# Performance work log

Measured on AMD Instinct MI355X. Metric: run time of the kernel, lower is better.

Reference implementation:

```python
import jax, jax.numpy as jnp
import numpy as np

D = 256   # hidden_dim
N = 1024  # total nodes
NP = 384  # paratope nodes
NE = 384  # epitope nodes
NC = 14   # atom channels


def setup_inputs() -> dict:
    key = jax.random.key(0)
    ks = jax.random.split(key, 24)
    s = 1.0 / np.sqrt(D)
    s3 = 1.0 / np.sqrt(3 * D)
    w = lambda k, shape, sc: (jax.random.normal(k, shape, jnp.float32) * sc)
    z = lambda: jnp.zeros((D,), jnp.float32)
    return {
        "H": w(ks[0], (N, D), 1.0),
        "X": w(ks[1], (N, NC, 3), 1.0),
        "paratope_mask": jnp.zeros((N,), bool).at[:NP].set(True),
        "epitope_mask": jnp.zeros((N,), bool).at[NP:NP + NE].set(True),
        "res_w1": w(ks[2], (1, D), 1.0), "res_b1": z(),
        "res_w2": w(ks[3], (D, D), s), "res_b2": z(),
        "atom_w1": w(ks[4], (1, D), 1.0), "atom_b1": z(),
        "atom_w2": w(ks[5], (D, D), s), "atom_b2": z(),
        "sim_weight": jnp.float32(0.5),
        "int_w1": w(ks[6], (3 * D, D), s3), "int_b1": z(),
        "int_w2": w(ks[7], (D, D), s), "int_b2": z(),
        "wl": w(ks[8], (D, D), s),
        "wr": w(ks[9], (D, D), s),
        "wg_w": w(ks[10], (D, D), s), "wg_b": z(),
        "wq_w": w(ks[11], (D, D), s), "wq_b": z(),
        "wk_w": w(ks[12], (D, D), s), "wk_b": z(),
        "wv_w": w(ks[13], (D, D), s), "wv_b": z(),
    }


def _mlp2(x, w1, b1, w2, b2):
    return jax.nn.silu(x @ w1 + b1) @ w2 + b2


def reference(H, X, paratope_mask, epitope_mask,
              res_w1, res_b1, res_w2, res_b2,
              atom_w1, atom_b1, atom_w2, atom_b2,
              sim_weight,
              int_w1, int_b1, int_w2, int_b2,
              wl, wr, wg_w, wg_b, wq_w, wq_b, wk_w, wk_b, wv_w, wv_b):
    p_idx = jnp.nonzero(paratope_mask, size=NP)[0]
    e_idx = jnp.nonzero(epitope_mask, size=NE)[0]
    Hp = H[p_idx]                      # [NP, D]
    He = H[e_idx]                      # [NE, D]
    Xp_ca = X[p_idx, 1]                # [NP, 3] (CA atom)
    Xe_ca = X[e_idx, 1]                # [NE, 3]

    dX = Xp_ca[:, None, :] - Xe_ca[None, :, :]         # [NP, NE, 3]
    S = jnp.sum(dX * dX, axis=-1, keepdims=True)       # [NP, NE, 1]
    # original computes S_residue and S_atom with identical formula
    S_res = _mlp2(S, res_w1, res_b1, res_w2, res_b2)
    S_atom = _mlp2(S, atom_w1, atom_b1, atom_w2, atom_b2)
    wmix = jax.nn.sigmoid(sim_weight)
    S_comb = wmix * S_res + (1.0 - wmix) * S_atom      # [NP, NE, D]

    Hp_e = jnp.broadcast_to(Hp[:, None, :], (NP, NE, D))
    He_e = jnp.broadcast_to(He[None, :, :], (NP, NE, D))
    Z_in = jnp.concatenate([Hp_e, He_e, S_comb], axis=-1)  # [NP, NE, 3D]
    Z = _mlp2(Z_in, int_w1, int_b1, int_w2, int_b2)        # [NP, NE, D]

    I = (Hp @ wl)[:, None, :] * (He @ wr)[None, :, :]      # outer-product interaction
    gate = jax.nn.sigmoid(Z @ wg_w + wg_b)
    f_tri = gate * I

    Q = Z @ wq_w + wq_b
    K = Z @ wk_w + wk_b
    V = Z @ wv_w + wv_b
    scores = jnp.einsum('ped,pfd->pef', Q, K) / (D ** 0.5)  # [NP, NE, NE]
    A = jax.nn.softmax(scores, axis=-1)
    f_att = jnp.einsum('pef,pfd->ped', A, V)

    H_tri = f_tri + f_att                                   # [NP, NE, D]
    return H.at[p_idx].set(H_tri.mean(axis=1))
```

## Files before the change

### kernel.cpp

```cpp
#include <hip/hip_runtime.h>

#define NPAR 384
#define NEPI 384
#define DD   256
#define NTAB 4096
#define SMAX 96.0f
#define SDELTA (SMAX / NTAB)
#define SINVD (NTAB / SMAX)

using bf16x8 = __bf16 __attribute__((ext_vector_type(8)));
using bf16x2 = __bf16 __attribute__((ext_vector_type(2)));
using f32x4  = float __attribute__((ext_vector_type(4)));

#if defined(__has_builtin)
#if __has_builtin(__builtin_amdgcn_cvt_pk_bf16_f32)
#define HAVE_PK_BF16 1
#endif
#if __has_builtin(__builtin_amdgcn_rcpf)
#define HAVE_RCPF 1
#endif
#endif

__device__ __forceinline__ float fastrcp(float x) {
#ifdef HAVE_RCPF
  return __builtin_amdgcn_rcpf(x);
#else
  return 1.0f / x;
#endif
}
__device__ __forceinline__ float sigm(float x) { return fastrcp(1.0f + __expf(-x)); }
__device__ __forceinline__ float silu(float x) { return x * fastrcp(1.0f + __expf(-x)); }
__device__ __forceinline__ unsigned short f2bf(float f) {
  unsigned u = __float_as_uint(f);
  u += 0x7fffu + ((u >> 16) & 1u);
  return (unsigned short)(u >> 16);
}
__device__ __forceinline__ float bf2f(unsigned u16) {
  return __uint_as_float(u16 << 16);
}
__device__ __forceinline__ uint2 pack4(float a, float b, float c, float d) {
  uint2 r;
#ifdef HAVE_PK_BF16
  bf16x2 lo = __builtin_amdgcn_cvt_pk_bf16_f32(a, b);
  bf16x2 hi = __builtin_amdgcn_cvt_pk_bf16_f32(c, d);
  r.x = __builtin_bit_cast(unsigned, lo);
  r.y = __builtin_bit_cast(unsigned, hi);
#else
  r.x = (unsigned)f2bf(a) | ((unsigned)f2bf(b) << 16);
  r.y = (unsigned)f2bf(c) | ((unsigned)f2bf(d) << 16);
#endif
  return r;
}

__device__ __forceinline__ void store_packed(unsigned short* __restrict__ wp,
                                             int slot, int k, int n, float v) {
  const int ks = k >> 5, lhi = (k >> 3) & 3, j = k & 7;
  const int tile = n >> 4, llo = n & 15;
  const int lane = lhi * 16 + llo;
  wp[slot * 65536 + (((ks * 16 + tile) * 64 + lane) << 3) + j] = f2bf(v);
}


__global__ void prep_kernel(
    const float* __restrict__ H, const float* __restrict__ wl,
    const float* __restrict__ wr, const float* __restrict__ int_w1,
    const float* __restrict__ res_w2, const float* __restrict__ atom_w2,
    const float* __restrict__ res_b2, const float* __restrict__ atom_b2,
    const float* __restrict__ int_b1, const float* __restrict__ simw,
    const float* __restrict__ wq_b, const float* __restrict__ wk_w,
    const float* __restrict__ wq_w, const float* __restrict__ int_w2,
    const float* __restrict__ wg_w,
    float* __restrict__ Hpl, float* __restrict__ Her,
    float* __restrict__ P1, float* __restrict__ P2,
    float* __restrict__ cvec, float* __restrict__ gv,
    unsigned short* __restrict__ wpack) {
  __shared__ float sbuf[1024];
  const int b = blockIdx.x, t = threadIdx.x;
  if (b < 256) {
    const bool isMa = b >= 128;
    const int i0 = (b & 127) * 2;
    const float wmix = 1.0f / (1.0f + __expf(-simw[0]));
    const float sc = isMa ? (1.0f - wmix) : wmix;
    const float* W2 = isMa ? atom_w2 : res_w2;
    sbuf[t] = W2[i0 * 256 + t];
    sbuf[256 + t] = W2[(i0 + 1) * 256 + t];
    __syncthreads();
    float a0 = 0.f, a1 = 0.f;
#pragma unroll 8
    for (int k = 0; k < 256; ++k) {
      const float w = int_w1[(512 + k) * 256 + t];
      a0 = fmaf(sbuf[k], w, a0);
      a1 = fmaf(sbuf[256 + k], w, a1);
    }
    const int slot = isMa ? 1 : 0;
    store_packed(wpack, slot, i0, t, a0 * sc);
    store_packed(wpack, slot, i0 + 1, t, a1 * sc);
  } else if (b == 256) {
    const float wmix = 1.0f / (1.0f + __expf(-simw[0]));
    float acc = int_b1[t];
#pragma unroll 8
    for (int k = 0; k < 256; ++k) {
      float bm = wmix * res_b2[k] + (1.0f - wmix) * atom_b2[k];
      acc += bm * int_w1[(512 + k) * 256 + t];
    }
    cvec[t] = acc;
  } else if (b < 321) {
    const int lane = t & 63, w = t >> 6;
    const int d = (b - 257) * 4 + w;
    float acc = 0.f;
#pragma unroll
    for (int i = 0; i < 4; ++i) {
      const int c = i * 64 + lane;
      acc += wk_w[d * 256 + c] * wq_b[c];
    }
    acc += __shfl_xor(acc, 1);
    acc += __shfl_xor(acc, 2);
    acc += __shfl_xor(acc, 4);
    acc += __shfl_xor(acc, 8);
    acc += __shfl_xor(acc, 16);
    acc += __shfl_xor(acc, 32);
    if (lane == 0) gv[d] = acc;
  } else if (b < 577) {
    const int r = b - 321;
    sbuf[t] = wq_w[r * 256 + t];
    __syncthreads();
    const float* wkrow = wk_w + t * 256;
    float a0 = 0.f, a1 = 0.f, a2 = 0.f, a3 = 0.f;
#pragma unroll 4
    for (int k = 0; k < 256; k += 4) {
      const f32x4 wv4 = *reinterpret_cast<const f32x4*>(&wkrow[k]);
      a0 = fmaf(sbuf[k + 0], wv4[0], a0);
      a1 = fmaf(sbuf[k + 1], wv4[1], a1);
      a2 = fmaf(sbuf[k + 2], wv4[2], a2);
      a3 = fmaf(sbuf[k + 3], wv4[3], a3);
    }
    store_packed(wpack, 4, r, t, (a0 + a1) + (a2 + a3));
  } else if (b < 961) {
    const int idx = b - 577;
    const int seg = idx / 96, r0 = (idx % 96) * 4;
    const float* A;
    const float* B;
    float* C;
    switch (seg) {
      case 0:  A = H + r0 * 256;            B = wl;              C = Hpl + r0 * 256; break;
      case 1:  A = H + (NPAR + r0) * 256;   B = wr;              C = Her + r0 * 256; break;
      case 2:  A = H + r0 * 256;            B = int_w1;          C = P1 + r0 * 256;  break;
      default: A = H + (NPAR + r0) * 256;   B = int_w1 + 65536;  C = P2 + r0 * 256;  break;
    }
#pragma unroll
    for (int j = 0; j < 4; ++j) sbuf[j * 256 + t] = A[j * 256 + t];
    __syncthreads();
    float a0 = 0.f, a1 = 0.f, a2 = 0.f, a3 = 0.f;
#pragma unroll 8
    for (int k = 0; k < 256; ++k) {
      const float bv = B[k * 256 + t];
      a0 = fmaf(sbuf[k], bv, a0);
      a1 = fmaf(sbuf[256 + k], bv, a1);
      a2 = fmaf(sbuf[512 + k], bv, a2);
      a3 = fmaf(sbuf[768 + k], bv, a3);
    }
    C[t] = a0;
    C[256 + t] = a1;
    C[512 + t] = a2;
    C[768 + t] = a3;
  } else {
    const int idx = (b - 961) * 256 + t;
    const int m = idx >> 16;
    const int r = idx & 65535;
    const int chunk = r >> 9;
    const int lane = (r >> 3) & 63;
    const int j = r & 7;
    const int k = (chunk >> 4) * 32 + (lane >> 4) * 8 + j;
    const int n = (chunk & 15) * 16 + (lane & 15);
    const float* src = (m == 0) ? int_w2 : wg_w;
    wpack[(2 + m) * 65536 + r] = f2bf(src[k * 256 + n]);
  }
}


__device__ __forceinline__ void zero_acc4(f32x4 (&acc)[4][4]) {
#pragma unroll
  for (int mt = 0; mt < 4; ++mt)
#pragma unroll
    for (int nt = 0; nt < 4; ++nt)
      acc[mt][nt] = (f32x4){0.f, 0.f, 0.f, 0.f};
}

__device__ __forceinline__ void gemm4(f32x4 (&acc)[4][4],
                                      const unsigned short* __restrict__ wp,
                                      const unsigned short* ub, int lane, int wv) {
  const int l15 = lane & 15, l4 = lane >> 4;
#pragma unroll
  for (int ks = 0; ks < 8; ++ks) {
    bf16x8 a[4];
#pragma unroll
    for (int mt = 0; mt < 4; ++mt)
      a[mt] = *reinterpret_cast<const bf16x8*>(wp + ((ks * 16 + wv * 4 + mt) * 64 + lane) * 8);
    __builtin_amdgcn_s_setprio(1);
#pragma unroll
    for (int nt = 0; nt < 4; ++nt) {
      bf16x8 b = *reinterpret_cast<const bf16x8*>(ub + (nt * 16 + l15) * 264 + ks * 32 + l4 * 8);
#pragma unroll
      for (int mt = 0; mt < 4; ++mt)
        acc[mt][nt] = __builtin_amdgcn_mfma_f32_16x16x32_bf16(a[mt], b, acc[mt][nt], 0, 0, 0);
    }
    __builtin_amdgcn_s_setprio(0);
  }
}

__device__ __forceinline__ void fill_u(unsigned short* ub, const float* Sv,
                                       const float* __restrict__ w1,
                                       const float* __restrict__ b1, int t) {
  const int dg = t & 31, rb = t >> 5;
  const f32x4 w1a = *reinterpret_cast<const f32x4*>(&w1[dg * 8]);
  const f32x4 w1b = *reinterpret_cast<const f32x4*>(&w1[dg * 8 + 4]);
  const f32x4 b1a = *reinterpret_cast<const f32x4*>(&b1[dg * 8]);
  const f32x4 b1b = *reinterpret_cast<const f32x4*>(&b1[dg * 8 + 4]);
#pragma unroll
  for (int i = 0; i < 8; ++i) {
    const int e = rb + i * 8;
    const float s = Sv[e];
    uint2 lo = pack4(silu(fmaf(s, w1a[0], b1a[0])), silu(fmaf(s, w1a[1], b1a[1])),
                     silu(fmaf(s, w1a[2], b1a[2])), silu(fmaf(s, w1a[3], b1a[3])));
    uint2 hi = pack4(silu(fmaf(s, w1b[0], b1b[0])), silu(fmaf(s, w1b[1], b1b[1])),
                     silu(fmaf(s, w1b[2], b1b[2])), silu(fmaf(s, w1b[3], b1b[3])));
    uint4 pk = {lo.x, lo.y, hi.x, hi.y};
    *reinterpret_cast<uint4*>(&ub[e * 264 + dg * 8]) = pk;
  }
}


__global__ __launch_bounds__(256, 3) void tab_kernel(
    const float* __restrict__ res_w1, const float* __restrict__ res_b1,
    const float* __restrict__ atom_w1, const float* __restrict__ atom_b1,
    const unsigned short* __restrict__ wpack, float* __restrict__ tabF) {
  __shared__ __align__(16) unsigned short ubuf[64 * 264];
  __shared__ float Sv[64];
  const int t = threadIdx.x, lane = t & 63, wv = t >> 6;
  const int l15 = lane & 15, l4 = lane >> 4;
  const int n0 = blockIdx.x * 64;
  if (t < 64) Sv[t] = (n0 + t) * SDELTA;
  __syncthreads();
  f32x4 acc[4][4];
  zero_acc4(acc);
  fill_u(ubuf, Sv, res_w1, res_b1, t);
  __syncthreads();
  gemm4(acc, wpack + 0 * 65536, ubuf, lane, wv);
  __syncthreads();
  fill_u(ubuf, Sv, atom_w1, atom_b1, t);
  __syncthreads();
  gemm4(acc, wpack + 1 * 65536, ubuf, lane, wv);
#pragma unroll
  for (int mt = 0; mt < 4; ++mt) {
    const int d = wv * 64 + mt * 16 + l4 * 4;
#pragma unroll
    for (int nt = 0; nt < 4; ++nt) {
      const int n = n0 + nt * 16 + l15;
      *reinterpret_cast<f32x4*>(&tabF[n * 256 + d]) = acc[mt][nt];
    }
  }
}


__global__ __launch_bounds__(256, 4) void pair_kernel(
    const float* __restrict__ Xg, const float* __restrict__ tabF,
    const float* __restrict__ int_b2, const float* __restrict__ wg_b,
    const unsigned short* __restrict__ wpack, const float* __restrict__ cvec,
    const float* __restrict__ P1, const float* __restrict__ P2,
    const float* __restrict__ Hpl, const float* __restrict__ Her,
    float* __restrict__ ftri, unsigned short* __restrict__ Zsw) {
  __shared__ __align__(16) unsigned short ubuf[64 * 264];
  __shared__ float Sv[64];
  __shared__ float pc[DD];
  const int t = threadIdx.x, lane = t & 63, wv = t >> 6;
  const int l15 = lane & 15, l4 = lane >> 4;
  const int wg = (blockIdx.x & 7) * 288 + (blockIdx.x >> 3);
  const int p = wg / 6, cc = wg % 6, e0 = cc * 64;
  const int d0 = wv * 64;

  if (t < 64) {
    const int e = e0 + t;
    float dx = Xg[p * 42 + 3] - Xg[(NPAR + e) * 42 + 3];
    float dy = Xg[p * 42 + 4] - Xg[(NPAR + e) * 42 + 4];
    float dz = Xg[p * 42 + 5] - Xg[(NPAR + e) * 42 + 5];
    Sv[t] = dx * dx + dy * dy + dz * dz;
  }
  pc[t] = P1[p * DD + t] + cvec[t];
  __syncthreads();

  {
    const int dg = t & 31, rb = t >> 5;
    const f32x4 pca = *reinterpret_cast<const f32x4*>(&pc[dg * 8]);
    const f32x4 pcb = *reinterpret_cast<const f32x4*>(&pc[dg * 8 + 4]);
#pragma unroll
    for (int i = 0; i < 8; ++i) {
      const int e = rb + i * 8;
      float sv = Sv[e] * SINVD;
      int idx = (int)sv;
      idx = idx > (NTAB - 2) ? (NTAB - 2) : idx;
      const float fr = sv - (float)idx;
      const f32x4 t0a = *reinterpret_cast<const f32x4*>(&tabF[idx * 256 + dg * 8]);
      const f32x4 t0b = *reinterpret_cast<const f32x4*>(&tabF[idx * 256 + dg * 8 + 4]);
      const f32x4 t1a = *reinterpret_cast<const f32x4*>(&tabF[(idx + 1) * 256 + dg * 8]);
      const f32x4 t1b = *reinterpret_cast<const f32x4*>(&tabF[(idx + 1) * 256 + dg * 8 + 4]);
      const f32x4 p2a = *reinterpret_cast<const f32x4*>(&P2[(e0 + e) * DD + dg * 8]);
      const f32x4 p2b = *reinterpret_cast<const f32x4*>(&P2[(e0 + e) * DD + dg * 8 + 4]);
      float z0 = fmaf(fr, t1a[0] - t0a[0], t0a[0]) + pca[0] + p2a[0];
      float z1 = fmaf(fr, t1a[1] - t0a[1], t0a[1]) + pca[1] + p2a[1];
      float z2 = fmaf(fr, t1a[2] - t0a[2], t0a[2]) + pca[2] + p2a[2];
      float z3 = fmaf(fr, t1a[3] - t0a[3], t0a[3]) + pca[3] + p2a[3];
      float z4 = fmaf(fr, t1b[0] - t0b[0], t0b[0]) + pcb[0] + p2b[0];
      float z5 = fmaf(fr, t1b[1] - t0b[1], t0b[1]) + pcb[1] + p2b[1];
      float z6 = fmaf(fr, t1b[2] - t0b[2], t0b[2]) + pcb[2] + p2b[2];
      float z7 = fmaf(fr, t1b[3] - t0b[3], t0b[3]) + pcb[3] + p2b[3];
      uint2 lo = pack4(silu(z0), silu(z1), silu(z2), silu(z3));
      uint2 hi = pack4(silu(z4), silu(z5), silu(z6), silu(z7));
      uint4 pk = {lo.x, lo.y, hi.x, hi.y};
      *reinterpret_cast<uint4*>(&ubuf[e * 264 + dg * 8]) = pk;
    }
  }
  __syncthreads();

  f32x4 acc[4][4];
  zero_acc4(acc);
  gemm4(acc, wpack + 2 * 65536, ubuf, lane, wv);
  __syncthreads();
#pragma unroll
  for (int mt = 0; mt < 4; ++mt) {
    const int d = d0 + mt * 16 + l4 * 4;
    const f32x4 bb = *reinterpret_cast<const f32x4*>(&int_b2[d]);
#pragma unroll
    for (int nt = 0; nt < 4; ++nt) {
      const int e = nt * 16 + l15;
      *reinterpret_cast<uint2*>(&ubuf[e * 264 + d]) =
          pack4(acc[mt][nt][0] + bb[0], acc[mt][nt][1] + bb[1],
                acc[mt][nt][2] + bb[2], acc[mt][nt][3] + bb[3]);
    }
  }
  __syncthreads();

  {
    unsigned short* Zd = Zsw + (size_t)p * 98304 + (size_t)(cc * 4 + wv) * 4096 + lane * 8;
#pragma unroll
    for (int ks = 0; ks < 8; ++ks) {
      *reinterpret_cast<uint4*>(Zd + ks * 512) =
          *reinterpret_cast<const uint4*>(&ubuf[(wv * 16 + l15) * 264 + ks * 32 + l4 * 8]);
    }
  }

  zero_acc4(acc);
  gemm4(acc, wpack + 3 * 65536, ubuf, lane, wv);
#pragma unroll
  for (int mt = 0; mt < 4; ++mt) {
    const int d = d0 + mt * 16 + l4 * 4;
    const f32x4 bb = *reinterpret_cast<const f32x4*>(&wg_b[d]);
    const f32x4 hl = *reinterpret_cast<const f32x4*>(&Hpl[p * DD + d]);
    f32x4 fs = (f32x4){0.f, 0.f, 0.f, 0.f};
#pragma unroll
    for (int nt = 0; nt < 4; ++nt) {
      const int e = e0 + nt * 16 + l15;
      const f32x4 hr = *reinterpret_cast<const f32x4*>(&Her[e * DD + d]);
#pragma unroll
      for (int r = 0; r < 4; ++r)
        fs[r] += sigm(acc[mt][nt][r] + bb[r]) * hr[r];
    }
#pragma unroll
    for (int r = 0; r < 4; ++r) {
      float v = fs[r] * hl[r];
      v += __shfl_xor(v, 1);
      v += __shfl_xor(v, 2);
      v += __shfl_xor(v, 4);
      v += __shfl_xor(v, 8);
      if (l15 == 0) atomicAdd(&ftri[p * DD + d + r], v);
    }
  }
}


__global__ __launch_bounds__(256, 4) void attn_kernel(
    const unsigned short* __restrict__ Zsw, const float* __restrict__ gv,
    const unsigned short* __restrict__ wpack, float* __restrict__ cbufg) {
  __shared__ __align__(16) unsigned short Tc[32 * 264];
  __shared__ float red[128];
  __shared__ float red2[128];
  const int t = threadIdx.x, lane = t & 63, wv = t >> 6;
  const int l15 = lane & 15, l4 = lane >> 4;
  const int xcd = blockIdx.x & 7, inner = blockIdx.x >> 3;
  const int p = (inner / 12) * 8 + xcd, c = inner % 12;
  const unsigned short* Zsp = Zsw + (size_t)p * 98304;
  const unsigned short* wqk = wpack + 4 * 65536;

  {
    f32x4 ta[4][2];
#pragma unroll
    for (int mt = 0; mt < 4; ++mt)
#pragma unroll
      for (int nt = 0; nt < 2; ++nt) ta[mt][nt] = (f32x4){0.f, 0.f, 0.f, 0.f};
    const unsigned short* Tb = Zsp + (size_t)(c * 2) * 4096 + lane * 8;
    bf16x8 bcur[2], bnxt[2];
#pragma unroll
    for (int nt = 0; nt < 2; ++nt)
      bcur[nt] = *reinterpret_cast<const bf16x8*>(Tb + nt * 4096);
#pragma unroll
    for (int ks = 0; ks < 8; ++ks) {
      if (ks < 7) {
#pragma unroll
        for (int nt = 0; nt < 2; ++nt)
          bnxt[nt] = *reinterpret_cast<const bf16x8*>(Tb + nt * 4096 + (ks + 1) * 512);
      }
      bf16x8 a[4];
#pragma unroll
      for (int mt = 0; mt < 4; ++mt)
        a[mt] = *reinterpret_cast<const bf16x8*>(wqk + ((ks * 16 + wv * 4 + mt) * 64 + lane) * 8);
      __builtin_amdgcn_s_setprio(1);
#pragma unroll
      for (int nt = 0; nt < 2; ++nt)
#pragma unroll
        for (int mt = 0; mt < 4; ++mt)
          ta[mt][nt] = __builtin_amdgcn_mfma_f32_16x16x32_bf16(a[mt], bcur[nt], ta[mt][nt], 0, 0, 0);
      __builtin_amdgcn_s_setprio(0);
      if (ks < 7) {
#pragma unroll
        for (int nt = 0; nt < 2; ++nt) bcur[nt] = bnxt[nt];
      }
    }
#pragma unroll
    for (int mt = 0; mt < 4; ++mt) {
      const int d = wv * 64 + mt * 16 + l4 * 4;
      const f32x4 gq = *reinterpret_cast<const f32x4*>(&gv[d]);
#pragma unroll
      for (int nt = 0; nt < 2; ++nt) {
        const int e = nt * 16 + l15;
        *reinterpret_cast<uint2*>(&Tc[e * 264 + d]) =
            pack4((ta[mt][nt][0] + gq[0]) * 0.0625f, (ta[mt][nt][1] + gq[1]) * 0.0625f,
                  (ta[mt][nt][2] + gq[2]) * 0.0625f, (ta[mt][nt][3] + gq[3]) * 0.0625f);
      }
    }
  }
  __syncthreads();

  f32x4 sc[2][6];
#pragma unroll
  for (int mt = 0; mt < 2; ++mt)
#pragma unroll
    for (int s = 0; s < 6; ++s) sc[mt][s] = (f32x4){0.f, 0.f, 0.f, 0.f};

  {
    const unsigned short* Sb = Zsp + (size_t)wv * 4096 + lane * 8;
    bf16x8 b0[3], b1[3];
#pragma unroll
    for (int j = 0; j < 3; ++j)
      b0[j] = *reinterpret_cast<const bf16x8*>(Sb + j * 16384);
#pragma unroll
    for (int ks = 0; ks < 8; ++ks) {
#pragma unroll
      for (int j = 0; j < 3; ++j)
        b1[j] = *reinterpret_cast<const bf16x8*>(Sb + (3 + j) * 16384 + ks * 512);
      bf16x8 a[2];
#pragma unroll
      for (int mt = 0; mt < 2; ++mt)
        a[mt] = *reinterpret_cast<const bf16x8*>(&Tc[(mt * 16 + l15) * 264 + ks * 32 + l4 * 8]);
      __builtin_amdgcn_s_setprio(1);
#pragma unroll
      for (int j = 0; j < 3; ++j)
#pragma unroll
        for (int mt = 0; mt < 2; ++mt)
          sc[mt][j] = __builtin_amdgcn_mfma_f32_16x16x32_bf16(a[mt], b0[j], sc[mt][j], 0, 0, 0);
      __builtin_amdgcn_s_setprio(0);
      if (ks < 7) {
#pragma unroll
        for (int j = 0; j < 3; ++j)
          b0[j] = *reinterpret_cast<const bf16x8*>(Sb + j * 16384 + (ks + 1) * 512);
      }
      __builtin_amdgcn_s_setprio(1);
#pragma unroll
      for (int j = 0; j < 3; ++j)
#pragma unroll
        for (int mt = 0; mt < 2; ++mt)
          sc[mt][3 + j] = __builtin_amdgcn_mfma_f32_16x16x32_bf16(a[mt], b1[j], sc[mt][3 + j], 0, 0, 0);
      __builtin_amdgcn_s_setprio(0);
    }
  }

  float rmax[2][4];
#pragma unroll
  for (int mt = 0; mt < 2; ++mt) {
#pragma unroll
    for (int r = 0; r < 4; ++r) {
      float m = -1e30f;
#pragma unroll
      for (int s = 0; s < 6; ++s) m = fmaxf(m, sc[mt][s][r]);
      m = fmaxf(m, __shfl_xor(m, 1));
      m = fmaxf(m, __shfl_xor(m, 2));
      m = fmaxf(m, __shfl_xor(m, 4));
      m = fmaxf(m, __shfl_xor(m, 8));
      rmax[mt][r] = m;
    }
  }
  if (l15 == 0) {
#pragma unroll
    for (int mt = 0; mt < 2; ++mt)
#pragma unroll
      for (int r = 0; r < 4; ++r)
        red[wv * 32 + mt * 16 + l4 * 4 + r] = rmax[mt][r];
  }
  __syncthreads();
#pragma unroll
  for (int mt = 0; mt < 2; ++mt) {
#pragma unroll
    for (int r = 0; r < 4; ++r) {
      const int row = mt * 16 + l4 * 4 + r;
      rmax[mt][r] = fmaxf(fmaxf(red[row], red[32 + row]), fmaxf(red[64 + row], red[96 + row]));
    }
  }

  float rsum[2][4];
#pragma unroll
  for (int mt = 0; mt < 2; ++mt) {
#pragma unroll
    for (int r = 0; r < 4; ++r) {
      float sSum = 0.f;
#pragma unroll
      for (int s = 0; s < 6; ++s) {
        float e = __expf(sc[mt][s][r] - rmax[mt][r]);
        sc[mt][s][r] = e;
        sSum += e;
      }
      sSum += __shfl_xor(sSum, 1);
      sSum += __shfl_xor(sSum, 2);
      sSum += __shfl_xor(sSum, 4);
      sSum += __shfl_xor(sSum, 8);
      rsum[mt][r] = sSum;
    }
  }
  if (l15 == 0) {
#pragma unroll
    for (int mt = 0; mt < 2; ++mt)
#pragma unroll
      for (int r = 0; r < 4; ++r)
        red2[wv * 32 + mt * 16 + l4 * 4 + r] = rsum[mt][r];
  }
  __syncthreads();
  float rinv[2][4];
#pragma unroll
  for (int mt = 0; mt < 2; ++mt) {
#pragma unroll
    for (int r = 0; r < 4; ++r) {
      const int row = mt * 16 + l4 * 4 + r;
      rinv[mt][r] = fastrcp(red2[row] + red2[32 + row] + red2[64 + row] + red2[96 + row]);
    }
  }

#pragma unroll
  for (int s = 0; s < 6; ++s) {
    float v = 0.f;
#pragma unroll
    for (int mt = 0; mt < 2; ++mt)
#pragma unroll
      for (int r = 0; r < 4; ++r)
        v += sc[mt][s][r] * rinv[mt][r];
    v += __shfl_xor(v, 16);
    v += __shfl_xor(v, 32);
    if (lane < 16)
      atomicAdd(&cbufg[p * NEPI + (s * 4 + wv) * 16 + lane], v);
  }
}


__global__ __launch_bounds__(256) void outa_kernel(
    const unsigned short* __restrict__ Zsw, const float* __restrict__ cbufg,
    float* __restrict__ ubufg) {
  __shared__ float cb[128];
  __shared__ float part[16][257];
  const int p = blockIdx.x / 3, th = blockIdx.x % 3, g0 = th * 8;
  const int t = threadIdx.x;
  const int lane = t & 63, wv = t >> 6;
  const int l15 = lane & 15, l4 = lane >> 4;
  if (t < 128) cb[t] = cbufg[p * NEPI + g0 * 16 + t];
  __syncthreads();
  const unsigned short* Zsp = Zsw + (size_t)p * 98304;
  float a16[16];
#pragma unroll
  for (int j = 0; j < 16; ++j) a16[j] = 0.f;
#pragma unroll
  for (int gr = 0; gr < 8; ++gr) {
    const int grp = g0 + gr;
    const float w = cb[gr * 16 + l15];
    const uint4 z0 = *reinterpret_cast<const uint4*>(Zsp + grp * 4096 + wv * 512 + lane * 8);
    const uint4 z1 = *reinterpret_cast<const uint4*>(Zsp + grp * 4096 + (wv + 4) * 512 + lane * 8);
    a16[0] = fmaf(w, bf2f(z0.x & 0xffffu), a16[0]);
    a16[1] = fmaf(w, bf2f(z0.x >> 16), a16[1]);
    a16[2] = fmaf(w, bf2f(z0.y & 0xffffu), a16[2]);
    a16[3] = fmaf(w, bf2f(z0.y >> 16), a16[3]);
    a16[4] = fmaf(w, bf2f(z0.z & 0xffffu), a16[4]);
    a16[5] = fmaf(w, bf2f(z0.z >> 16), a16[5]);
    a16[6] = fmaf(w, bf2f(z0.w & 0xffffu), a16[6]);
    a16[7] = fmaf(w, bf2f(z0.w >> 16), a16[7]);
    a16[8]  = fmaf(w, bf2f(z1.x & 0xffffu), a16[8]);
    a16[9]  = fmaf(w, bf2f(z1.x >> 16), a16[9]);
    a16[10] = fmaf(w, bf2f(z1.y & 0xffffu), a16[10]);
    a16[11] = fmaf(w, bf2f(z1.y >> 16), a16[11]);
    a16[12] = fmaf(w, bf2f(z1.z & 0xffffu), a16[12]);
    a16[13] = fmaf(w, bf2f(z1.z >> 16), a16[13]);
    a16[14] = fmaf(w, bf2f(z1.w & 0xffffu), a16[14]);
    a16[15] = fmaf(w, bf2f(z1.w >> 16), a16[15]);
  }
#pragma unroll
  for (int j = 0; j < 8; ++j) part[l15][wv * 32 + l4 * 8 + j] = a16[j];
#pragma unroll
  for (int j = 0; j < 8; ++j) part[l15][128 + wv * 32 + l4 * 8 + j] = a16[8 + j];
  __syncthreads();
  float uu = 0.f;
#pragma unroll
  for (int g = 0; g < 16; ++g) uu += part[g][t];
  atomicAdd(&ubufg[p * DD + t], uu);
}


__global__ __launch_bounds__(256) void out2_kernel(
    const float* __restrict__ ubufg, const float* __restrict__ ftri,
    const float* __restrict__ wvw, const float* __restrict__ wvb,
    float* __restrict__ out) {
  __shared__ float u[DD];
  const int p = blockIdx.x, t = threadIdx.x;
  u[t] = ubufg[p * DD + t];
  __syncthreads();
  float acc = ftri[p * DD + t] + 384.0f * wvb[t];
#pragma unroll 8
  for (int d = 0; d < DD; ++d)
    acc = fmaf(u[d], wvw[d * DD + t], acc);
  out[p * DD + t] = acc * (1.0f / 384.0f);
}


extern "C" void kernel_launch(void* const* d_in, const int* in_sizes, int n_in,
                              void* d_out, int out_size, void* d_ws, size_t ws_size,
                              hipStream_t stream) {
  (void)in_sizes; (void)n_in; (void)out_size; (void)ws_size;
  const float* H = (const float*)d_in[0];
  const float* X = (const float*)d_in[1];
  const float* res_w1 = (const float*)d_in[4];
  const float* res_b1 = (const float*)d_in[5];
  const float* res_w2 = (const float*)d_in[6];
  const float* res_b2 = (const float*)d_in[7];
  const float* atom_w1 = (const float*)d_in[8];
  const float* atom_b1 = (const float*)d_in[9];
  const float* atom_w2 = (const float*)d_in[10];
  const float* atom_b2 = (const float*)d_in[11];
  const float* simw = (const float*)d_in[12];
  const float* int_w1 = (const float*)d_in[13];
  const float* int_b1 = (const float*)d_in[14];
  const float* int_w2 = (const float*)d_in[15];
  const float* int_b2 = (const float*)d_in[16];
  const float* wl = (const float*)d_in[17];
  const float* wr = (const float*)d_in[18];
  const float* wg_w = (const float*)d_in[19];
  const float* wg_b = (const float*)d_in[20];
  const float* wq_w = (const float*)d_in[21];
  const float* wq_b = (const float*)d_in[22];
  const float* wk_w = (const float*)d_in[23];
  const float* wv_w = (const float*)d_in[25];
  const float* wv_b = (const float*)d_in[26];

  char* ws = (char*)d_ws;
  unsigned short* wpack = (unsigned short*)(ws + 0);
  float* cvec  = (float*)(ws + 655360);
  float* gv    = (float*)(ws + 656384);
  float* P1    = (float*)(ws + 657408);
  float* P2    = (float*)(ws + 1050624);
  float* Hpl   = (float*)(ws + 1443840);
  float* Her   = (float*)(ws + 1837056);
  float* ftri  = (float*)(ws + 2230272);
  float* cbufg = (float*)(ws + 2623488);
  float* ubufg = (float*)(ws + 3213312);
  unsigned short* Zsw = (unsigned short*)(ws + 3606528);
  float* tabF  = (float*)(ws + 79104000);

  hipMemsetAsync(ftri, 0, 393216 + 589824 + 393216, stream);
  prep_kernel<<<1473, 256, 0, stream>>>(H, wl, wr, int_w1, res_w2, atom_w2,
                                        res_b2, atom_b2, int_b1, simw, wq_b, wk_w,
                                        wq_w, int_w2, wg_w,
                                        Hpl, Her, P1, P2, cvec, gv, wpack);
  tab_kernel<<<NTAB / 64, 256, 0, stream>>>(res_w1, res_b1, atom_w1, atom_b1, wpack, tabF);
  pair_kernel<<<2304, 256, 0, stream>>>(X, tabF, int_b2, wg_b, wpack, cvec,
                                        P1, P2, Hpl, Her, ftri, Zsw);
  attn_kernel<<<4608, 256, 0, stream>>>(Zsw, gv, wpack, cbufg);
  outa_kernel<<<1152, 256, 0, stream>>>(Zsw, cbufg, ubufg);
  out2_kernel<<<384, 256, 0, stream>>>(ubufg, ftri, wv_w, wv_b, (float*)d_out);
  hipMemcpyAsync((float*)d_out + NPAR * DD, H + NPAR * DD,
                 (1024 - NPAR) * DD * sizeof(float), hipMemcpyDeviceToDevice, stream);
}
```

Measured before the change: 312.0 us.

## Prefetch full next k-slice in attention, drop pc smem staging, move memcpy first

The attention score loop now prefetches all six B fragments for the next k-step into a second register set and issues all twelve MFMAs per step together, replacing the split half-prefetch scheme. In pair_kernel, the per-row P1+cvec vector is read straight from global memory into registers instead of being staged through shared memory. The tail device-to-device copy of untouched H rows is moved to the start of the stream. Together these aim to hide load latency and trim shared memory use, at the cost of more VGPRs, which may reduce occupancy.

```diff
diff --git a/kernel.cpp b/kernel.cpp
--- a/kernel.cpp
+++ b/kernel.cpp
@@ -271,7 +271,6 @@
     float* __restrict__ ftri, unsigned short* __restrict__ Zsw) {
   __shared__ __align__(16) unsigned short ubuf[64 * 264];
   __shared__ float Sv[64];
-  __shared__ float pc[DD];
   const int t = threadIdx.x, lane = t & 63, wv = t >> 6;
   const int l15 = lane & 15, l4 = lane >> 4;
   const int wg = (blockIdx.x & 7) * 288 + (blockIdx.x >> 3);
@@ -285,13 +284,16 @@
     float dz = Xg[p * 42 + 5] - Xg[(NPAR + e) * 42 + 5];
     Sv[t] = dx * dx + dy * dy + dz * dz;
   }
-  pc[t] = P1[p * DD + t] + cvec[t];
   __syncthreads();
 
   {
     const int dg = t & 31, rb = t >> 5;
-    const f32x4 pca = *reinterpret_cast<const f32x4*>(&pc[dg * 8]);
-    const f32x4 pcb = *reinterpret_cast<const f32x4*>(&pc[dg * 8 + 4]);
+    const f32x4 p1a = *reinterpret_cast<const f32x4*>(&P1[p * DD + dg * 8]);
+    const f32x4 p1b = *reinterpret_cast<const f32x4*>(&P1[p * DD + dg * 8 + 4]);
+    const f32x4 cva = *reinterpret_cast<const f32x4*>(&cvec[dg * 8]);
+    const f32x4 cvb = *reinterpret_cast<const f32x4*>(&cvec[dg * 8 + 4]);
+    const f32x4 pca = p1a + cva;
+    const f32x4 pcb = p1b + cvb;
 #pragma unroll
     for (int i = 0; i < 8; ++i) {
       const int e = rb + i * 8;
@@ -447,38 +449,32 @@
 
   {
     const unsigned short* Sb = Zsp + (size_t)wv * 4096 + lane * 8;
-    bf16x8 b0[3], b1[3];
-#pragma unroll
-    for (int j = 0; j < 3; ++j)
-      b0[j] = *reinterpret_cast<const bf16x8*>(Sb + j * 16384);
+    bf16x8 bc[6], bn[6];
+#pragma unroll
+    for (int j = 0; j < 6; ++j)
+      bc[j] = *reinterpret_cast<const bf16x8*>(Sb + j * 16384);
 #pragma unroll
     for (int ks = 0; ks < 8; ++ks) {
-#pragma unroll
-      for (int j = 0; j < 3; ++j)
-        b1[j] = *reinterpret_cast<const bf16x8*>(Sb + (3 + j) * 16384 + ks * 512);
+      if (ks < 7) {
+#pragma unroll
+        for (int j = 0; j < 6; ++j)
+          bn[j] = *reinterpret_cast<const bf16x8*>(Sb + j * 16384 + (ks + 1) * 512);
+      }
       bf16x8 a[2];
 #pragma unroll
       for (int mt = 0; mt < 2; ++mt)
         a[mt] = *reinterpret_cast<const bf16x8*>(&Tc[(mt * 16 + l15) * 264 + ks * 32 + l4 * 8]);
       __builtin_amdgcn_s_setprio(1);
 #pragma unroll
-      for (int j = 0; j < 3; ++j)
+      for (int j = 0; j < 6; ++j)
 #pragma unroll
         for (int mt = 0; mt < 2; ++mt)
-          sc[mt][j] = __builtin_amdgcn_mfma_f32_16x16x32_bf16(a[mt], b0[j], sc[mt][j], 0, 0, 0);
+          sc[mt][j] = __builtin_amdgcn_mfma_f32_16x16x32_bf16(a[mt], bc[j], sc[mt][j], 0, 0, 0);
       __builtin_amdgcn_s_setprio(0);
       if (ks < 7) {
 #pragma unroll
-        for (int j = 0; j < 3; ++j)
-          b0[j] = *reinterpret_cast<const bf16x8*>(Sb + j * 16384 + (ks + 1) * 512);
+        for (int j = 0; j < 6; ++j) bc[j] = bn[j];
       }
-      __builtin_amdgcn_s_setprio(1);
-#pragma unroll
-      for (int j = 0; j < 3; ++j)
-#pragma unroll
-        for (int mt = 0; mt < 2; ++mt)
-          sc[mt][3 + j] = __builtin_amdgcn_mfma_f32_16x16x32_bf16(a[mt], b1[j], sc[mt][3 + j], 0, 0, 0);
-      __builtin_amdgcn_s_setprio(0);
     }
   }
 
@@ -676,6 +672,8 @@
   unsigned short* Zsw = (unsigned short*)(ws + 3606528);
   float* tabF  = (float*)(ws + 79104000);
 
+  hipMemcpyAsync((float*)d_out + NPAR * DD, H + NPAR * DD,
+                 (1024 - NPAR) * DD * sizeof(float), hipMemcpyDeviceToDevice, stream);
   hipMemsetAsync(ftri, 0, 393216 + 589824 + 393216, stream);
   prep_kernel<<<1473, 256, 0, stream>>>(H, wl, wr, int_w1, res_w2, atom_w2,
                                         res_b2, atom_b2, int_b1, simw, wq_b, wk_w,
@@ -687,6 +685,4 @@
   attn_kernel<<<4608, 256, 0, stream>>>(Zsw, gv, wpack, cbufg);
   outa_kernel<<<1152, 256, 0, stream>>>(Zsw, cbufg, ubufg);
   out2_kernel<<<384, 256, 0, stream>>>(ubufg, ftri, wv_w, wv_b, (float*)d_out);
-  hipMemcpyAsync((float*)d_out + NPAR * DD, H + NPAR * DD,
-                 (1024 - NPAR) * DD * sizeof(float), hipMemcpyDeviceToDevice, stream);
-}
+}
```

Measured after the change: 320.3 us. 1.03x slower.
